# Kernel optimization log

Measured on AMD Instinct MI355X. Metric: run time of the kernel, lower is better.

The kernel has to match this reference:

```python
import jax, jax.numpy as jnp
import numpy as np

N_VERTS = 2562


def _uniform(key, shape, bound):
    return jax.random.uniform(key, shape, jnp.float32, -bound, bound)


def vert_align(feat, pos):
    # feat: [B,C,H,W]; pos: [B,N,3], xy in [-1,1] -> bilinear sample -> [B,N,C]
    B, C, H, W = feat.shape
    ft = jnp.transpose(feat, (0, 2, 3, 1))  # [B,H,W,C]
    x = (jnp.clip(pos[..., 0], -1.0, 1.0) + 1.0) * 0.5 * (W - 1)
    y = (jnp.clip(pos[..., 1], -1.0, 1.0) + 1.0) * 0.5 * (H - 1)
    x0 = jnp.floor(x)
    y0 = jnp.floor(y)
    x0i = x0.astype(jnp.int32)
    y0i = y0.astype(jnp.int32)
    x1i = jnp.minimum(x0i + 1, W - 1)
    y1i = jnp.minimum(y0i + 1, H - 1)
    wx = (x - x0)[..., None]
    wy = (y - y0)[..., None]
    b = jnp.arange(B)[:, None]
    f00 = ft[b, y0i, x0i]
    f01 = ft[b, y0i, x1i]
    f10 = ft[b, y1i, x0i]
    f11 = ft[b, y1i, x1i]
    return (f00 * (1 - wx) * (1 - wy) + f01 * wx * (1 - wy)
            + f10 * (1 - wx) * wy + f11 * wx * wy)


def graph_conv(x, adj, w0, w1):
    # relu(x @ w0 + adj @ (x @ w1))
    return jax.nn.relu(x @ w0 + jnp.einsum('bij,bjc->bic', adj, x @ w1))


def setup_inputs() -> dict:
    key = jax.random.key(0)
    ks = jax.random.split(key, 20)
    B, N = 8, N_VERTS
    inp = {
        'conv2_3': jax.random.normal(ks[0], (B, 256, 56, 56), jnp.float32),
        'conv3_4': jax.random.normal(ks[1], (B, 512, 28, 28), jnp.float32),
        'conv4_6': jax.random.normal(ks[2], (B, 1024, 14, 14), jnp.float32),
        'conv5_3': jax.random.normal(ks[3], (B, 2048, 7, 7), jnp.float32),
        # scaled so row sums are O(1), like a normalized dense adjacency
        'vertex_adjacency': jax.random.uniform(ks[4], (B, N, N), jnp.float32) * (2.0 / N),
        'vertex_positions': jax.random.uniform(ks[5], (B, N, 3), jnp.float32) * 2.0 - 1.0,
        'vertex_features': jax.random.normal(ks[6], (B, N, 128), jnp.float32),
    }
    # learned parameters (torch default / GraphConv uniform init)
    inp['w_lin0'] = _uniform(ks[7], (3840, 128), 1.0 / np.sqrt(3840))
    inp['b_lin0'] = _uniform(ks[8], (128,), 1.0 / np.sqrt(3840))
    inp['gc0_w0'] = _uniform(ks[9], (259, 131), 1.0 / np.sqrt(259))
    inp['gc0_w1'] = _uniform(ks[10], (259, 131), 1.0 / np.sqrt(259))
    inp['gc1_w0'] = _uniform(ks[11], (131, 128), 1.0 / np.sqrt(131))
    inp['gc1_w1'] = _uniform(ks[12], (131, 128), 1.0 / np.sqrt(131))
    inp['gc2_w0'] = _uniform(ks[13], (131, 128), 1.0 / np.sqrt(131))
    inp['gc2_w1'] = _uniform(ks[14], (131, 128), 1.0 / np.sqrt(131))
    inp['w_lin1'] = _uniform(ks[15], (128, 3), 1.0 / np.sqrt(128))
    inp['b_lin1'] = _uniform(ks[16], (3,), 1.0 / np.sqrt(128))
    return inp


def reference(conv2_3, conv3_4, conv4_6, conv5_3, vertex_adjacency,
              vertex_positions, vertex_features,
              w_lin0, b_lin0, gc0_w0, gc0_w1, gc1_w0, gc1_w1,
              gc2_w0, gc2_w1, w_lin1, b_lin1):
    verts = jnp.concatenate(
        [vert_align(f, vertex_positions)
         for f in (conv2_3, conv3_4, conv4_6, conv5_3)], axis=2)  # [B,N,3840]
    projected = verts @ w_lin0 + b_lin0                             # [B,N,128]
    vf = jnp.concatenate([vertex_features, vertex_positions, projected], axis=2)  # 259
    h = graph_conv(vf, vertex_adjacency, gc0_w0, gc0_w1)            # [B,N,131]
    h = jnp.concatenate([vertex_positions, h], axis=2)              # 134? no: 3+131=134 -- see note
    h = graph_conv(h[:, :, :131] if h.shape[2] != 131 else h, vertex_adjacency, gc1_w0, gc1_w1)
    h = jnp.concatenate([vertex_positions, h], axis=2)              # 131
    new_features = graph_conv(h, vertex_adjacency, gc2_w0, gc2_w1)  # [B,N,128]
    new_positions = vertex_positions + jnp.tanh(new_features @ w_lin1 + b_lin1)
    return new_positions, new_features
```

## Files before the change

### kernel.cpp

```cpp
#include <hip/hip_runtime.h>
#include <hip/hip_bf16.h>

typedef __attribute__((ext_vector_type(8))) short bf16x8;
typedef __attribute__((ext_vector_type(4))) float f32x4;
typedef long long i64;

static __device__ __forceinline__ float bflo(unsigned v){ return __uint_as_float(v << 16); }
static __device__ __forceinline__ float bfhi(unsigned v){ return __uint_as_float(v & 0xffff0000u); }
static __device__ __forceinline__ unsigned short f2bf(float f){
  unsigned u = __float_as_uint(f);
  u += 0x7FFFu + ((u >> 16) & 1u);
  return (unsigned short)(u >> 16);
}
static __device__ __forceinline__ unsigned f2e4m3(float x){
  unsigned b = __float_as_uint(x);
  unsigned s = (b >> 31) << 7;
  b &= 0x7fffffffu;
  if (b >= 0x43e80000u) return s | 0x7eu;
  if (b < 0x3c800000u)
    return s | (unsigned)rintf(__uint_as_float(b) * 512.f);
  unsigned b2 = b + 0x7ffffu + ((b >> 20) & 1u);
  return s | (((b2 >> 23) - 120u) << 3) | ((b2 >> 20) & 7u);
}
static __device__ __forceinline__ void gload_lds16(const void* g, void* l){
  __builtin_amdgcn_global_load_lds((const __attribute__((address_space(1))) unsigned int*)g,
                                   (__attribute__((address_space(3))) unsigned int*)l, 16, 0, 0);
}

#define MFMA16(acc, a, b) (acc) = __builtin_amdgcn_mfma_f32_16x16x32_bf16((a),(b),(acc),0,0,0)
#define MFMA8(acc, a, b)  (acc) = __builtin_amdgcn_mfma_f32_16x16x32_fp8_fp8((a),(b),(acc),0,0,0)

#define NB    8
#define NVRT  2562
#define MP    2624
#define NRB2  82
#define NRB16 164
#define NKT8  21
#define KOCT  336
#define YO    ((size_t)KOCT*128*8)

#define G_B0 0ul
#define G_B1 3211264ul
#define G_B2 4014080ul
#define G_B3 4214784ul
#define G_TOT 4264960ul

struct PWArgs {
  const float* src[7];
  unsigned short* dst[7];
  int ksrc[7], nsrc[7];
};
__global__ void k_packw_all(PWArgs a)
{
  const int cb[8] = {0,491520,528384,565248,585728,606208,626688,647168};
  int g = blockIdx.x * 256 + threadIdx.x;
#pragma unroll
  for (int s = 0; s < 7; s++){
    if (g >= cb[s] && g < cb[s+1]){
      int li = g - cb[s];
      int k = li >> 7, c = li & 127;
      int ks = a.ksrc[s], ns = a.nsrc[s];
      float v = (k < ks) ? a.src[s][(size_t)k * ns + c] : 0.f;
      a.dst[s][((size_t)(k >> 3) * 128 + c) * 8 + (k & 7)] = f2bf(v);
    }
  }
}

__global__ __launch_bounds__(256) void k_gproj2(
    const float* __restrict__ c0m, const float* __restrict__ c1m,
    const float* __restrict__ c2m, const float* __restrict__ c3m,
    const unsigned short* __restrict__ wp,
    unsigned short* __restrict__ G)
{
  __shared__ f32x4 red[3][1024];
  int bx = blockIdx.x;
  int m, b, tile;
  if (bx < 784)      { m = 0; b = bx / 98;  tile = bx - b*98; }
  else if (bx < 984) { int l = bx-784;  m = 1; b = l / 25; tile = l - b*25; }
  else if (bx < 1040){ int l = bx-984;  m = 2; b = l / 7;  tile = l - b*7; }
  else               { int l = bx-1040; m = 3; b = l >> 1; tile = l & 1; }
  int C  = 256 << m;
  int HW = (m==0)?3136:(m==1)?784:(m==2)?196:49;
  const float* src = ((m==0)?c0m:(m==1)?c1m:(m==2)?c2m:c3m) + (size_t)b * C * HW;
  size_t gb = ((m==0)?G_B0:(m==1)?G_B1:(m==2)?G_B2:G_B3) + (size_t)b * HW * 128;
  int ko8 = (m==0)?0:(m==1)?32:(m==2)?96:224;

  int t = threadIdx.x, w = t >> 6, lane = t & 63;
  int l15 = lane & 15, l4 = lane >> 4;
  int hw0 = tile * 32;
  int ar0 = min(hw0 + l15, HW - 1);
  int ar1 = min(hw0 + 16 + l15, HW - 1);

  f32x4 acc[2][8];
#pragma unroll
  for (int i = 0; i < 2; i++)
#pragma unroll
    for (int j = 0; j < 8; j++) acc[i][j] = (f32x4){0,0,0,0};

  int kq = C >> 2;
  int kbeg = w * kq, klim = kbeg + kq;
  for (int kb = kbeg; kb < klim; kb += 32){
    bf16x8 a0, a1;
#pragma unroll
    for (int j = 0; j < 8; j++){
      int cc = kb + l4*8 + j;
      a0[j] = (short)f2bf(src[(size_t)cc * HW + ar0]);
      a1[j] = (short)f2bf(src[(size_t)cc * HW + ar1]);
    }
    size_t bo = ((size_t)(ko8 + (kb>>3) + l4) * 128 + l15) * 8;
#pragma unroll
    for (int cf = 0; cf < 8; cf++){
      bf16x8 bb = *(const bf16x8*)(wp + bo + cf*128);
      MFMA16(acc[0][cf], a0, bb);
      MFMA16(acc[1][cf], a1, bb);
    }
  }

  if (w){
#pragma unroll
    for (int rf = 0; rf < 2; rf++)
#pragma unroll
      for (int cf = 0; cf < 8; cf++)
        red[w-1][(rf*8+cf)*64 + lane] = acc[rf][cf];
  }
  __syncthreads();
  if (!w){
#pragma unroll
    for (int rf = 0; rf < 2; rf++)
#pragma unroll
      for (int cf = 0; cf < 8; cf++){
        int i = (rf*8+cf)*64 + lane;
        f32x4 s = acc[rf][cf] + red[0][i] + red[1][i] + red[2][i];
        int col = cf*16 + l15;
#pragma unroll
        for (int r = 0; r < 4; r++){
          int hw = hw0 + rf*16 + l4*4 + r;
          if (hw < HW) G[gb + (size_t)hw*128 + col] = f2bf(s[r]);
        }
      }
  }
}

__global__ void k_prep2(const float* __restrict__ vfeat, const float* __restrict__ pos,
                        const unsigned short* __restrict__ G,
                        const float* __restrict__ bias,
                        unsigned short* __restrict__ vf,
                        unsigned short* __restrict__ x1,
                        unsigned short* __restrict__ x2,
                        unsigned char* __restrict__ y1A,
                        unsigned char* __restrict__ y1B)
{
  int b = blockIdx.y;
  if (blockIdx.x == 0){
    unsigned long long* za = (unsigned long long*)(y1A + (size_t)b*YO + (size_t)328*128*8);
    unsigned long long* zb = (unsigned long long*)(y1B + (size_t)b*YO + (size_t)328*128*8);
    int i = threadIdx.x;
#pragma unroll
    for (int j = 0; j < 4; j++){ za[i*4+j] = 0; zb[i*4+j] = 0; }
  }
  int row = blockIdx.x * 4 + (threadIdx.x >> 6);
  int lane = threadIdx.x & 63;
  size_t vfo = ((size_t)b * MP + row) * 288;
  size_t xo  = ((size_t)b * MP + row) * 160;
  if (row < NVRT){
    size_t src = (size_t)b * NVRT + row;
    float px = fminf(fmaxf(pos[src*3 + 0], -1.f), 1.f);
    float py = fminf(fmaxf(pos[src*3 + 1], -1.f), 1.f);
    int c0 = lane * 2;
    float s0 = bias[c0], s1 = bias[c0 + 1];
#pragma unroll
    for (int m = 0; m < 4; m++){
      int W = 56 >> m;
      int HW = W * W;
      size_t gb = (m==0)?G_B0:(m==1)?G_B1:(m==2)?G_B2:G_B3;
      float gx = (px + 1.f) * 0.5f * (float)(W - 1);
      float gy = (py + 1.f) * 0.5f * (float)(W - 1);
      int x0 = (int)floorf(gx), y0 = (int)floorf(gy);
      float wx = gx - (float)x0, wy = gy - (float)y0;
      int x1i = min(x0 + 1, W - 1), y1i = min(y0 + 1, W - 1);
      const unsigned short* g = G + gb + (size_t)b * HW * 128;
      unsigned v00 = *(const unsigned*)(g + ((size_t)(y0 *W + x0 ))*128 + c0);
      unsigned v01 = *(const unsigned*)(g + ((size_t)(y0 *W + x1i))*128 + c0);
      unsigned v10 = *(const unsigned*)(g + ((size_t)(y1i*W + x0 ))*128 + c0);
      unsigned v11 = *(const unsigned*)(g + ((size_t)(y1i*W + x1i))*128 + c0);
      float w00 = (1.f-wx)*(1.f-wy), w01 = wx*(1.f-wy);
      float w10 = (1.f-wx)*wy,       w11 = wx*wy;
      s0 += w00*bflo(v00) + w01*bflo(v01) + w10*bflo(v10) + w11*bflo(v11);
      s1 += w00*bfhi(v00) + w01*bfhi(v01) + w10*bfhi(v10) + w11*bfhi(v11);
    }
    vf[vfo + 131 + c0]     = f2bf(s0);
    vf[vfo + 131 + c0 + 1] = f2bf(s1);
    float2 fv = *(const float2*)(vfeat + src*128 + c0);
    vf[vfo + c0]     = f2bf(fv.x);
    vf[vfo + c0 + 1] = f2bf(fv.y);
    if (lane < 3){
      unsigned short v = f2bf(pos[src*3 + lane]);
      vf[vfo + 128 + lane] = v;
      x1[xo + lane] = v;
      x2[xo + lane] = v;
    }
    if (lane >= 32 && lane < 61) vf[vfo + 259 + (lane - 32)] = 0;
    if (lane < 29){ x1[xo + 131 + lane] = 0; x2[xo + 131 + lane] = 0; }
  } else {
    for (int c = lane; c < 288; c += 64) vf[vfo + c] = 0;
    for (int c = lane; c < 160; c += 64){ x1[xo + c] = 0; x2[xo + c] = 0; }
  }
}

template<int KX>
__global__ __launch_bounds__(256) void k_y1(
    const unsigned short* __restrict__ x,
    const unsigned short* __restrict__ wp1,
    unsigned char* __restrict__ y1p8)
{
  int b = blockIdx.y, rb = blockIdx.x * 32;
  int t = threadIdx.x, wave = t >> 6, lane = t & 63;
  int rf = wave & 1, ch = wave >> 1;
  int l15 = lane & 15, l4 = lane >> 4;
  f32x4 a1[4];
#pragma unroll
  for (int c = 0; c < 4; c++) a1[c] = (f32x4){0,0,0,0};
  int row = rb + rf*16 + l15;
  const unsigned short* xp = x + ((size_t)b * MP + row) * KX + l4 * 8;
#pragma unroll
  for (int kb = 0; kb < KX; kb += 32){
    bf16x8 a = *(const bf16x8*)(xp + kb);
    size_t bo = ((size_t)((kb>>3) + l4) * 128 + ch*64 + l15) * 8;
#pragma unroll
    for (int c = 0; c < 4; c++){
      bf16x8 b1 = *(const bf16x8*)(wp1 + bo + c*128);
      MFMA16(a1[c], a, b1);
    }
  }
  unsigned char* yb = y1p8 + (size_t)b * YO;
#pragma unroll
  for (int c = 0; c < 4; c++){
    int col = ch*64 + c*16 + l15;
    int orow0 = rb + rf*16 + l4*4;
    unsigned q = f2e4m3(a1[c][0]) | (f2e4m3(a1[c][1]) << 8)
               | (f2e4m3(a1[c][2]) << 16) | (f2e4m3(a1[c][3]) << 24);
    *(unsigned*)(yb + ((size_t)(orow0 >> 3) * 128 + col) * 8 + (orow0 & 7)) = q;
  }
}

__global__ __launch_bounds__(256) void k_adjfuse(
    const float* __restrict__ adj,
    unsigned char* __restrict__ adjP,
    const unsigned char* __restrict__ y1in,
    const unsigned short* __restrict__ x,
    const unsigned short* __restrict__ wp0,
    const unsigned short* __restrict__ wp1n,
    unsigned char* __restrict__ y1out,
    const float* __restrict__ posg,
    unsigned short* __restrict__ xnext)
{
  __shared__ __align__(16) unsigned char abuf[2][2048];
  __shared__ unsigned short xbuf[16][168];
  int rb = blockIdx.x, b = blockIdx.y;
  int t = threadIdx.x, w = t >> 6, lane = t & 63;
  int l15 = lane & 15, l4 = lane >> 4;
  int r = t >> 4, kseg = t & 15;
  int grow = rb*16 + r;
  bool rv = grow < NVRT;
  const float* arow = adj + ((size_t)b*NVRT + (rv ? grow : 0))*NVRT;
  unsigned char* tb = adjP + (((size_t)b*NRB16 + rb)*NKT8) * 2048;
  int tslot = 128*r + 8*(kseg ^ r);
  const unsigned char* yb = y1in + (size_t)b * YO;

  f32x4 acc[2], accW[2];
  acc[0] = (f32x4){0,0,0,0};  acc[1] = (f32x4){0,0,0,0};
  accW[0] = (f32x4){0,0,0,0}; accW[1] = (f32x4){0,0,0,0};

  auto loadf32 = [&](int kt, float* v){
    int gk = kt*128 + kseg*8;
    if (rv && gk + 8 <= NVRT){
      float4 f0 = *(const float4*)(arow + gk);
      float4 f1 = *(const float4*)(arow + gk + 4);
      v[0]=f0.x; v[1]=f0.y; v[2]=f0.z; v[3]=f0.w;
      v[4]=f1.x; v[5]=f1.y; v[6]=f1.z; v[7]=f1.w;
    } else if (rv){
#pragma unroll
      for (int e = 0; e < 8; e++){ int k = gk + e; v[e] = (k < NVRT) ? arow[k] : 0.f; }
    } else {
#pragma unroll
      for (int e = 0; e < 8; e++) v[e] = 0.f;
    }
  };
  auto cvt = [&](const float* v)->unsigned long long {
    unsigned long long q = 0;
#pragma unroll
    for (int e = 0; e < 8; e++)
      q |= (unsigned long long)f2e4m3(v[e] * 1024.f) << (8*e);
    return q;
  };

  float v0[8];
  loadf32(0, v0);

  if (t < 48){
    int r16 = t / 3, c = t - r16*3;
    int g2 = rb*16 + r16;
    xbuf[r16][c] = (g2 < NVRT) ? f2bf(posg[((size_t)b*NVRT + g2)*3 + c]) : 0;
  }
  {
    int r16 = t >> 4, c0 = 131 + (t & 15);
    xbuf[r16][c0] = 0;
    if (c0 + 16 < 168) xbuf[r16][c0 + 16] = 0;
    if (c0 + 32 < 168) xbuf[r16][c0 + 32] = 0;
  }

  const unsigned short* xr = x + ((size_t)b*MP + rb*16 + l15)*288 + l4*8;
#pragma unroll
  for (int kb = 0; kb < 288; kb += 32){
    bf16x8 ax = *(const bf16x8*)(xr + kb);
    size_t bo = ((size_t)((kb>>3) + l4)*128 + w*32 + l15)*8;
    MFMA16(accW[0], ax, *(const bf16x8*)(wp0 + bo));
    MFMA16(accW[1], ax, *(const bf16x8*)(wp0 + bo + 128));
  }

  unsigned long long q = cvt(v0);
  float vn[8];

  for (int kt = 0; kt < NKT8; ++kt){
    int cur = kt & 1;
    *(unsigned long long*)(&abuf[cur][tslot]) = q;
    *(unsigned long long*)(tb + (size_t)kt*2048 + tslot) = q;
    if (kt < NKT8-1) loadf32(kt+1, vn);
    __syncthreads();
    const unsigned char* ab = &abuf[cur][0];
#pragma unroll
    for (int sel = 0; sel < 2; sel++){
#pragma unroll
      for (int ks = 0; ks < 2; ks++){
        int koct = sel*8 + ks*4 + l4;
        i64 a = *(const i64*)(ab + 128*l15 + 8*(koct ^ l15));
        const unsigned char* bp = yb + ((size_t)(kt*16 + koct)*128 + w*32 + l15)*8;
        i64 b0 = *(const i64*)(bp);
        i64 b1 = *(const i64*)(bp + 128);
        MFMA8(acc[0], a, b0);
        MFMA8(acc[1], a, b1);
      }
    }
    if (kt < NKT8-1) q = cvt(vn);
  }

#pragma unroll
  for (int cf = 0; cf < 2; cf++){
    int col = w*32 + cf*16 + l15;
#pragma unroll
    for (int rr = 0; rr < 4; rr++){
      int row16 = l4*4 + rr;
      int row = rb*16 + row16;
      float vv = fmaxf(accW[cf][rr] + acc[cf][rr] * 0.0009765625f, 0.f);
      unsigned short hb = f2bf(vv);
      if (row < NVRT) xnext[((size_t)b*MP + row)*160 + 3 + col] = hb;
      xbuf[row16][3 + col] = hb;
    }
  }
  __syncthreads();

  f32x4 accY[2];
  accY[0] = (f32x4){0,0,0,0}; accY[1] = (f32x4){0,0,0,0};
#pragma unroll
  for (int ks = 0; ks < 5; ks++){
    bf16x8 a = *(const bf16x8*)(&xbuf[l15][ks*32 + l4*8]);
    size_t bo = ((size_t)(ks*4 + l4)*128 + w*32 + l15)*8;
    MFMA16(accY[0], a, *(const bf16x8*)(wp1n + bo));
    MFMA16(accY[1], a, *(const bf16x8*)(wp1n + bo + 128));
  }
  unsigned char* yo = y1out + (size_t)b * YO;
#pragma unroll
  for (int cf = 0; cf < 2; cf++){
    int col = w*32 + cf*16 + l15;
    int orow0 = rb*16 + l4*4;
    unsigned qq = f2e4m3(accY[cf][0]) | (f2e4m3(accY[cf][1]) << 8)
                | (f2e4m3(accY[cf][2]) << 16) | (f2e4m3(accY[cf][3]) << 24);
    *(unsigned*)(yo + ((size_t)(orow0 >> 3) * 128 + col) * 8 + (orow0 & 7)) = qq;
  }
}

template<int EPI, int KX>
__global__ __launch_bounds__(256) void k_adj8(
    const unsigned char* __restrict__ adjP,
    const unsigned char* __restrict__ y1in,
    const unsigned short* __restrict__ x,
    const unsigned short* __restrict__ wp0,
    const unsigned short* __restrict__ wp1n,
    unsigned char* __restrict__ y1out,
    const float* __restrict__ posg,
    unsigned short* __restrict__ xnext,
    float* __restrict__ outf,
    const float* __restrict__ wl1, const float* __restrict__ bl1,
    float* __restrict__ opos)
{
  __shared__ __align__(16) unsigned char abuf[2][2048];
  __shared__ unsigned short xbuf[EPI == 0 ? 16 : 1][168];
  __shared__ float hbuf[EPI == 1 ? 16 : 1][128];
  int rb = blockIdx.x, b = blockIdx.y;
  int t = threadIdx.x, w = t >> 6, lane = t & 63;
  int l15 = lane & 15, l4 = lane >> 4;
  const unsigned char* tb = adjP + (((size_t)b*NRB16 + rb)*NKT8) * 2048;
  const unsigned char* yb = y1in + (size_t)b * YO;

  f32x4 acc[2], accW[2];
  acc[0] = (f32x4){0,0,0,0};  acc[1] = (f32x4){0,0,0,0};
  accW[0] = (f32x4){0,0,0,0}; accW[1] = (f32x4){0,0,0,0};

  auto stage = [&](int kt, int bufi){
    if (w < 2)
      gload_lds16(tb + (size_t)kt*2048 + w*1024 + lane*16, &abuf[bufi][w*1024]);
  };

  stage(0, 0);

  if (EPI == 0){
    if (t < 48){
      int r16 = t / 3, c = t - r16*3;
      int grow = rb*16 + r16;
      xbuf[r16][c] = (grow < NVRT) ? f2bf(posg[((size_t)b*NVRT + grow)*3 + c]) : 0;
    }
    {
      int r16 = t >> 4, c0 = 131 + (t & 15);
      xbuf[r16][c0] = 0;
      if (c0 + 16 < 168) xbuf[r16][c0 + 16] = 0;
      if (c0 + 32 < 168) xbuf[r16][c0 + 32] = 0;
    }
  }

  const unsigned short* xr = x + ((size_t)b*MP + rb*16 + l15)*KX + l4*8;
#pragma unroll
  for (int kb = 0; kb < KX; kb += 32){
    bf16x8 ax = *(const bf16x8*)(xr + kb);
    size_t bo = ((size_t)((kb>>3) + l4)*128 + w*32 + l15)*8;
    MFMA16(accW[0], ax, *(const bf16x8*)(wp0 + bo));
    MFMA16(accW[1], ax, *(const bf16x8*)(wp0 + bo + 128));
  }

  __syncthreads();

  for (int kt = 0; kt < NKT8; ++kt){
    int cur = kt & 1;
    if (kt < NKT8-1) stage(kt+1, cur ^ 1);
    const unsigned char* ab = &abuf[cur][0];
#pragma unroll
    for (int sel = 0; sel < 2; sel++){
#pragma unroll
      for (int ks = 0; ks < 2; ks++){
        int koct = sel*8 + ks*4 + l4;
        i64 a = *(const i64*)(ab + 128*l15 + 8*(koct ^ l15));
        const unsigned char* bp = yb + ((size_t)(kt*16 + koct)*128 + w*32 + l15)*8;
        i64 b0 = *(const i64*)(bp);
        i64 b1 = *(const i64*)(bp + 128);
        MFMA8(acc[0], a, b0);
        MFMA8(acc[1], a, b1);
      }
    }
    __syncthreads();
  }

#pragma unroll
  for (int cf = 0; cf < 2; cf++){
    int col = w*32 + cf*16 + l15;
#pragma unroll
    for (int r = 0; r < 4; r++){
      int row16 = l4*4 + r;
      int row = rb*16 + row16;
      float v = fmaxf(accW[cf][r] + acc[cf][r] * 0.0009765625f, 0.f);
      if (EPI == 0){
        unsigned short hb = f2bf(v);
        if (row < NVRT) xnext[((size_t)b*MP + row)*160 + 3 + col] = hb;
        xbuf[row16][3 + col] = hb;
      } else {
        if (row < NVRT) outf[((size_t)b*NVRT + row)*128 + col] = v;
        hbuf[row16][col] = v;
      }
    }
  }
  __syncthreads();

  if (EPI == 0){
    f32x4 accY[2];
    accY[0] = (f32x4){0,0,0,0}; accY[1] = (f32x4){0,0,0,0};
#pragma unroll
    for (int ks = 0; ks < 5; ks++){
      bf16x8 a = *(const bf16x8*)(&xbuf[l15][ks*32 + l4*8]);
      size_t bo = ((size_t)(ks*4 + l4)*128 + w*32 + l15)*8;
      MFMA16(accY[0], a, *(const bf16x8*)(wp1n + bo));
      MFMA16(accY[1], a, *(const bf16x8*)(wp1n + bo + 128));
    }
    unsigned char* yo = y1out + (size_t)b * YO;
#pragma unroll
    for (int cf = 0; cf < 2; cf++){
      int col = w*32 + cf*16 + l15;
      int orow0 = rb*16 + l4*4;
      unsigned q = f2e4m3(accY[cf][0]) | (f2e4m3(accY[cf][1]) << 8)
                 | (f2e4m3(accY[cf][2]) << 16) | (f2e4m3(accY[cf][3]) << 24);
      *(unsigned*)(yo + ((size_t)(orow0 >> 3) * 128 + col) * 8 + (orow0 & 7)) = q;
    }
  } else {
#pragma unroll
    for (int rr = 0; rr < 4; rr++){
      int row16 = w*4 + rr;
      int grow = rb*16 + row16;
      if (grow < NVRT){
        int c0 = lane * 2;
        float v0 = hbuf[row16][c0], v1 = hbuf[row16][c0+1];
        float p[3];
#pragma unroll
        for (int j = 0; j < 3; j++){
          p[j] = v0 * wl1[c0*3 + j] + v1 * wl1[c0*3 + 3 + j];
#pragma unroll
          for (int off = 1; off < 64; off <<= 1)
            p[j] += __shfl_xor(p[j], off);
        }
        if (lane == 0){
          size_t po = ((size_t)b * NVRT + grow) * 3;
#pragma unroll
          for (int j = 0; j < 3; j++)
            opos[po + j] = posg[po + j] + tanhf(p[j] + bl1[j]);
        }
      }
    }
  }
}

extern "C" void kernel_launch(void* const* d_in, const int* in_sizes, int n_in,
                              void* d_out, int out_size, void* d_ws, size_t ws_size,
                              hipStream_t stream)
{
  const float* conv[4] = {(const float*)d_in[0], (const float*)d_in[1],
                          (const float*)d_in[2], (const float*)d_in[3]};
  const float* adj   = (const float*)d_in[4];
  const float* pos   = (const float*)d_in[5];
  const float* vfeat = (const float*)d_in[6];
  const float* wlin0 = (const float*)d_in[7];
  const float* blin0 = (const float*)d_in[8];
  const float* gw[6] = {(const float*)d_in[9],  (const float*)d_in[10],
                        (const float*)d_in[11], (const float*)d_in[12],
                        (const float*)d_in[13], (const float*)d_in[14]};
  const float* wlin1 = (const float*)d_in[15];
  const float* blin1 = (const float*)d_in[16];

  char* ws = (char*)d_ws;
  size_t off = 0;
  auto take = [&](size_t bytes)->char* {
    char* p = ws + off;
    off += (bytes + 255) & ~(size_t)255;
    return p;
  };
  unsigned short* G    = (unsigned short*)take(G_TOT * 2);
  unsigned char*  adjP = (unsigned char*)take((size_t)NB*NRB16*NKT8*2048);
  unsigned short* wl0p = (unsigned short*)take((size_t)3840*128*2);
  unsigned short* w0p0 = (unsigned short*)take((size_t)288*128*2);
  unsigned short* w1p0 = (unsigned short*)take((size_t)288*128*2);
  unsigned short* w0p1 = (unsigned short*)take((size_t)160*128*2);
  unsigned short* w1p1 = (unsigned short*)take((size_t)160*128*2);
  unsigned short* w0p2 = (unsigned short*)take((size_t)160*128*2);
  unsigned short* w1p2 = (unsigned short*)take((size_t)160*128*2);
  unsigned short* vf   = (unsigned short*)take((size_t)NB*MP*288*2);
  unsigned short* x1   = (unsigned short*)take((size_t)NB*MP*160*2);
  unsigned short* x2   = (unsigned short*)take((size_t)NB*MP*160*2);
  unsigned char*  y1A  = (unsigned char*)take((size_t)NB*YO);
  unsigned char*  y1B  = (unsigned char*)take((size_t)NB*YO);

  float* out_pos  = (float*)d_out;
  float* out_feat = out_pos + (size_t)NB*NVRT*3;

  PWArgs pw;
  pw.src[0]=wlin0; pw.dst[0]=wl0p; pw.ksrc[0]=3840; pw.nsrc[0]=128;
  pw.src[1]=gw[0]; pw.dst[1]=w0p0; pw.ksrc[1]=259;  pw.nsrc[1]=131;
  pw.src[2]=gw[1]; pw.dst[2]=w1p0; pw.ksrc[2]=259;  pw.nsrc[2]=131;
  pw.src[3]=gw[2]; pw.dst[3]=w0p1; pw.ksrc[3]=131;  pw.nsrc[3]=128;
  pw.src[4]=gw[3]; pw.dst[4]=w1p1; pw.ksrc[4]=131;  pw.nsrc[4]=128;
  pw.src[5]=gw[4]; pw.dst[5]=w0p2; pw.ksrc[5]=131;  pw.nsrc[5]=128;
  pw.src[6]=gw[5]; pw.dst[6]=w1p2; pw.ksrc[6]=131;  pw.nsrc[6]=128;
  k_packw_all<<<2528, 256, 0, stream>>>(pw);
  k_gproj2<<<1056, 256, 0, stream>>>(conv[0], conv[1], conv[2], conv[3], wl0p, G);
  k_prep2<<<dim3(MP/4, NB), 256, 0, stream>>>(vfeat, pos, G, blin0, vf, x1, x2, y1A, y1B);
  k_y1<288><<<dim3(NRB2, NB), 256, 0, stream>>>(vf, w1p0, y1A);
  k_adjfuse<<<dim3(NRB16, NB), 256, 0, stream>>>(adj, adjP, y1A, vf, w0p0, w1p1, y1B, pos, x1);
  k_adj8<0,160><<<dim3(NRB16, NB), 256, 0, stream>>>(adjP, y1B, x1, w0p1, w1p2, y1A, pos,
                                                     x2, nullptr, nullptr, nullptr, nullptr);
  k_adj8<1,160><<<dim3(NRB16, NB), 256, 0, stream>>>(adjP, y1A, x2, w0p2, nullptr, nullptr, pos,
                                                     nullptr, out_feat, wlin1, blin1, out_pos);
  (void)in_sizes; (void)n_in; (void)out_size; (void)ws_size;
}
```

Before: 261.0 us.

## Batch adjacency tiles in adjfuse and preload whole adjacency row-block in adj8

In k_adjfuse, the K loop now handles three 128-wide adjacency tiles per stage, with fp32 loads two stages ahead and a single barrier per group of three. This replaces one barrier per tile and hides more global latency. In k_adj8, every fp8 adjacency tile of the row block is loaded into LDS up front, which removes all per-iteration barriers and double buffering. The cost is more LDS per block (NKT8*2KB) and more registers, which may lower occupancy. The adjfuse change hardcodes 7 groups of 3 tiles and so assumes NKT8 == 21.

```diff
diff --git a/kernel.cpp b/kernel.cpp
--- a/kernel.cpp
+++ b/kernel.cpp
@@ -254,7 +254,7 @@
     const float* __restrict__ posg,
     unsigned short* __restrict__ xnext)
 {
-  __shared__ __align__(16) unsigned char abuf[2][2048];
+  __shared__ __align__(16) unsigned char abuf[2][6144];
   __shared__ unsigned short xbuf[16][168];
   int rb = blockIdx.x, b = blockIdx.y;
   int t = threadIdx.x, w = t >> 6, lane = t & 63;
@@ -271,31 +271,26 @@
   acc[0] = (f32x4){0,0,0,0};  acc[1] = (f32x4){0,0,0,0};
   accW[0] = (f32x4){0,0,0,0}; accW[1] = (f32x4){0,0,0,0};
 
-  auto loadf32 = [&](int kt, float* v){
-    int gk = kt*128 + kseg*8;
+  float v[2][3][8];
+
+  auto loadf32 = [&](int ktg, float* vv){
+    int gk = ktg*128 + kseg*8;
     if (rv && gk + 8 <= NVRT){
       float4 f0 = *(const float4*)(arow + gk);
       float4 f1 = *(const float4*)(arow + gk + 4);
-      v[0]=f0.x; v[1]=f0.y; v[2]=f0.z; v[3]=f0.w;
-      v[4]=f1.x; v[5]=f1.y; v[6]=f1.z; v[7]=f1.w;
+      vv[0]=f0.x; vv[1]=f0.y; vv[2]=f0.z; vv[3]=f0.w;
+      vv[4]=f1.x; vv[5]=f1.y; vv[6]=f1.z; vv[7]=f1.w;
     } else if (rv){
 #pragma unroll
-      for (int e = 0; e < 8; e++){ int k = gk + e; v[e] = (k < NVRT) ? arow[k] : 0.f; }
+      for (int e = 0; e < 8; e++){ int k = gk + e; vv[e] = (k < NVRT) ? arow[k] : 0.f; }
     } else {
 #pragma unroll
-      for (int e = 0; e < 8; e++) v[e] = 0.f;
+      for (int e = 0; e < 8; e++) vv[e] = 0.f;
     }
   };
-  auto cvt = [&](const float* v)->unsigned long long {
-    unsigned long long q = 0;
-#pragma unroll
-    for (int e = 0; e < 8; e++)
-      q |= (unsigned long long)f2e4m3(v[e] * 1024.f) << (8*e);
-    return q;
-  };
-
-  float v0[8];
-  loadf32(0, v0);
+
+#pragma unroll
+  for (int j = 0; j < 3; j++) loadf32(j, v[0][j]);
 
   if (t < 48){
     int r16 = t / 3, c = t - r16*3;
@@ -318,30 +313,53 @@
     MFMA16(accW[1], ax, *(const bf16x8*)(wp0 + bo + 128));
   }
 
-  unsigned long long q = cvt(v0);
-  float vn[8];
-
-  for (int kt = 0; kt < NKT8; ++kt){
-    int cur = kt & 1;
-    *(unsigned long long*)(&abuf[cur][tslot]) = q;
-    *(unsigned long long*)(tb + (size_t)kt*2048 + tslot) = q;
-    if (kt < NKT8-1) loadf32(kt+1, vn);
+#pragma unroll
+  for (int j = 0; j < 3; j++){
+    unsigned long long q = 0;
+#pragma unroll
+    for (int e = 0; e < 8; e++)
+      q |= (unsigned long long)f2e4m3(v[0][j][e] * 1024.f) << (8*e);
+    *(unsigned long long*)(&abuf[0][j*2048 + tslot]) = q;
+    *(unsigned long long*)(tb + (size_t)j*2048 + tslot) = q;
+  }
+#pragma unroll
+  for (int j = 0; j < 3; j++) loadf32(3 + j, v[1][j]);
+  __syncthreads();
+
+#pragma unroll
+  for (int g = 0; g < 7; ++g){
+    const int cur = g & 1;
+    const unsigned char* ab = &abuf[cur][0];
+#pragma unroll
+    for (int j = 0; j < 3; j++){
+      int ktg = 3*g + j;
+#pragma unroll
+      for (int sel = 0; sel < 2; sel++)
+#pragma unroll
+        for (int ks = 0; ks < 2; ks++){
+          int koct = sel*8 + ks*4 + l4;
+          i64 a = *(const i64*)(ab + j*2048 + 128*l15 + 8*(koct ^ l15));
+          const unsigned char* bp = yb + ((size_t)(ktg*16 + koct)*128 + w*32 + l15)*8;
+          MFMA8(acc[0], a, *(const i64*)bp);
+          MFMA8(acc[1], a, *(const i64*)(bp + 128));
+        }
+    }
+    if (g < 6){
+#pragma unroll
+      for (int j = 0; j < 3; j++){
+        unsigned long long q = 0;
+#pragma unroll
+        for (int e = 0; e < 8; e++)
+          q |= (unsigned long long)f2e4m3(v[cur^1][j][e] * 1024.f) << (8*e);
+        *(unsigned long long*)(&abuf[cur^1][j*2048 + tslot]) = q;
+        *(unsigned long long*)(tb + (size_t)(3*(g+1) + j)*2048 + tslot) = q;
+      }
+      if (g < 5){
+#pragma unroll
+        for (int j = 0; j < 3; j++) loadf32(3*(g+2) + j, v[cur][j]);
+      }
+    }
     __syncthreads();
-    const unsigned char* ab = &abuf[cur][0];
-#pragma unroll
-    for (int sel = 0; sel < 2; sel++){
-#pragma unroll
-      for (int ks = 0; ks < 2; ks++){
-        int koct = sel*8 + ks*4 + l4;
-        i64 a = *(const i64*)(ab + 128*l15 + 8*(koct ^ l15));
-        const unsigned char* bp = yb + ((size_t)(kt*16 + koct)*128 + w*32 + l15)*8;
-        i64 b0 = *(const i64*)(bp);
-        i64 b1 = *(const i64*)(bp + 128);
-        MFMA8(acc[0], a, b0);
-        MFMA8(acc[1], a, b1);
-      }
-    }
-    if (kt < NKT8-1) q = cvt(vn);
   }
 
 #pragma unroll
@@ -393,7 +411,7 @@
     const float* __restrict__ wl1, const float* __restrict__ bl1,
     float* __restrict__ opos)
 {
-  __shared__ __align__(16) unsigned char abuf[2][2048];
+  __shared__ __align__(16) unsigned char abuf[NKT8 * 2048];
   __shared__ unsigned short xbuf[EPI == 0 ? 16 : 1][168];
   __shared__ float hbuf[EPI == 1 ? 16 : 1][128];
   int rb = blockIdx.x, b = blockIdx.y;
@@ -406,12 +424,11 @@
   acc[0] = (f32x4){0,0,0,0};  acc[1] = (f32x4){0,0,0,0};
   accW[0] = (f32x4){0,0,0,0}; accW[1] = (f32x4){0,0,0,0};
 
-  auto stage = [&](int kt, int bufi){
-    if (w < 2)
-      gload_lds16(tb + (size_t)kt*2048 + w*1024 + lane*16, &abuf[bufi][w*1024]);
-  };
-
-  stage(0, 0);
+  if (w < 2){
+#pragma unroll
+    for (int kt = 0; kt < NKT8; ++kt)
+      gload_lds16(tb + (size_t)kt*2048 + w*1024 + lane*16, &abuf[kt*2048 + w*1024]);
+  }
 
   if (EPI == 0){
     if (t < 48){
@@ -438,10 +455,9 @@
 
   __syncthreads();
 
+#pragma unroll 3
   for (int kt = 0; kt < NKT8; ++kt){
-    int cur = kt & 1;
-    if (kt < NKT8-1) stage(kt+1, cur ^ 1);
-    const unsigned char* ab = &abuf[cur][0];
+    const unsigned char* ab = &abuf[kt*2048];
 #pragma unroll
     for (int sel = 0; sel < 2; sel++){
 #pragma unroll
@@ -449,13 +465,10 @@
         int koct = sel*8 + ks*4 + l4;
         i64 a = *(const i64*)(ab + 128*l15 + 8*(koct ^ l15));
         const unsigned char* bp = yb + ((size_t)(kt*16 + koct)*128 + w*32 + l15)*8;
-        i64 b0 = *(const i64*)(bp);
-        i64 b1 = *(const i64*)(bp + 128);
-        MFMA8(acc[0], a, b0);
-        MFMA8(acc[1], a, b1);
+        MFMA8(acc[0], a, *(const i64*)bp);
+        MFMA8(acc[1], a, *(const i64*)(bp + 128));
       }
     }
-    __syncthreads();
   }
 
 #pragma unroll
```

New measurement: 273.7 us. 4.8% more time.
